# Kernel optimization log

Hardware: AMD Instinct MI355X
Metric: run time of the kernel (lower is better)

The kernel has to match this reference:

```python
import jax, jax.numpy as jnp
import numpy as np
import math

EPS = 1e-6


def setup_inputs() -> dict:
    key = jax.random.key(0)
    ks = jax.random.split(key, 6)
    Bsz, S, d_in, d_out, E, r = 4, 2048, 2048, 2048, 16, 16
    x = jax.random.normal(ks[0], (Bsz, S, d_in), dtype=jnp.float32)
    base_W = jax.random.normal(ks[1], (d_out, d_in), dtype=jnp.float32) * (1.0 / math.sqrt(d_in))
    base_b = jax.random.normal(ks[2], (d_out,), dtype=jnp.float32)
    A = jax.random.normal(ks[3], (E, r, d_in), dtype=jnp.float32) * (1.0 / math.sqrt(d_in))
    B = jax.random.normal(ks[4], (E, d_out, r), dtype=jnp.float32) * (1.0 / math.sqrt(r))
    gate_v = jax.random.normal(ks[5], (E, d_in), dtype=jnp.float32)
    alphas = jnp.full((E,), 32.0, dtype=jnp.float32)
    return {"x": x, "base_W": base_W, "base_b": base_b, "A": A, "B": B,
            "gate_v": gate_v, "alphas": alphas, "top_k": 2}


def reference(x, base_W, base_b, A, B, gate_v, alphas, top_k):
    d = x.shape[-1]
    out_shape = x.shape[:-1] + (base_W.shape[0],)
    base_out = jnp.einsum('bsd,od->bso', x, base_W) + base_b

    x_flat = x.reshape(-1, d)                                  # [T, d]
    T = x_flat.shape[0]
    E = A.shape[0]
    # cosine routing scores
    xn = x_flat / (jnp.linalg.norm(x_flat, axis=-1, keepdims=True) + EPS)
    vn = gate_v / (jnp.linalg.norm(gate_v, axis=-1, keepdims=True) + EPS)
    scores = (xn @ vn.T) / jnp.sqrt(jnp.float32(d))            # [T, E]
    topk_s, topk_i = jax.lax.top_k(scores, top_k)              # [T, k]
    w = jax.nn.softmax(topk_s, axis=-1)                        # [T, k]
    # dense combine weight per (token, expert); non-selected experts get 0
    Wte = jnp.zeros((T, E), dtype=x.dtype).at[jnp.arange(T)[:, None], topk_i].add(w)
    scale = alphas / jnp.float32(A.shape[1])                   # [E]
    # grouped LoRA: mid [T,E,r] is tiny (r=16); contract without [T,E,out]
    mid = jnp.einsum('td,erd->ter', x_flat, A)
    contrib = jnp.einsum('ter,eor,te,e->to', mid, B, Wte, scale)
    return base_out + contrib.reshape(out_shape)
```

## Files before the change

kernel.cpp:

```cpp
#include <hip/hip_runtime.h>
#include <math.h>


typedef unsigned short u16;
typedef __attribute__((ext_vector_type(8))) short short8;
typedef __attribute__((ext_vector_type(4))) float floatx4;

#define DEV __device__ __forceinline__

DEV u16 f2b(float f) { unsigned int u; __builtin_memcpy(&u, &f, 4); u += 0x7fffu + ((u >> 16) & 1u); return (u16)(u >> 16); }
DEV float ldf(const float* __restrict__ p, long long i, long long n) { if (i < 0 || i >= n) i = 0; return p[i]; }

DEV void async_cp16(const void* g, void* l) {
  __builtin_amdgcn_global_load_lds(
      (const __attribute__((address_space(1))) unsigned int*)g,
      (__attribute__((address_space(3))) unsigned int*)l, 16, 0, 0);
}

struct Route { int e0, e1; float c0, c1; };

#define MAX_T 8192
#define MAX_K 2048
#define MAX_DOUT 2048
#define MAX_ER 256

__device__ Route g_route[MAX_T];
__device__ float g_vnorm[16];
__device__ float g_mid[(size_t)MAX_T * MAX_ER];
__device__ __align__(16) u16 g_xb[(size_t)MAX_T * MAX_K];
__device__ __align__(16) u16 g_wb[(size_t)MAX_DOUT * MAX_K];
__device__ __align__(16) u16 g_ab[(size_t)MAX_ER * MAX_K];
__device__ __align__(16) u16 g_mw[(size_t)MAX_T * MAX_ER];
__device__ __align__(16) u16 g_w2[(size_t)MAX_DOUT * MAX_ER];

__global__ __launch_bounds__(256) void prep_all(
    const float* __restrict__ W, long long nW,
    const float* __restrict__ A, long long nA,
    const float* __restrict__ Bw, long long nB,
    const float* __restrict__ gv, long long nG,
    int d, int d_out, int r, int E, int Er,
    int nWblk, int nAblk, int w2blk) {
  int b = blockIdx.x;
  const int tid = threadIdx.x;
  if (b < nWblk) {
    const long long cap = (long long)MAX_DOUT * MAX_K;
    const long long stride = (long long)nWblk * 1024;
    for (long long i4 = ((long long)b * 256 + tid) * 4; i4 < nW; i4 += stride) {
      if (i4 + 4 <= nW && i4 + 4 <= cap) {
        const float4 v = *(const float4*)(W + i4);
        ushort4 o; o.x = f2b(v.x); o.y = f2b(v.y); o.z = f2b(v.z); o.w = f2b(v.w);
        *(ushort4*)&g_wb[i4] = o;
      } else {
        for (long long j = i4; j < nW && j < cap; ++j) g_wb[j] = f2b(W[j]);
      }
    }
    return;
  }
  b -= nWblk;
  if (b < nAblk) {
    const long long cap = (long long)MAX_ER * MAX_K;
    const long long stride = (long long)nAblk * 1024;
    for (long long i4 = ((long long)b * 256 + tid) * 4; i4 < nA; i4 += stride) {
      if (i4 + 4 <= nA && i4 + 4 <= cap) {
        const float4 v = *(const float4*)(A + i4);
        ushort4 o; o.x = f2b(v.x); o.y = f2b(v.y); o.z = f2b(v.z); o.w = f2b(v.w);
        *(ushort4*)&g_ab[i4] = o;
      } else {
        for (long long j = i4; j < nA && j < cap; ++j) g_ab[j] = f2b(A[j]);
      }
    }
    return;
  }
  b -= nAblk;
  if (b < w2blk) {
    const int gid = b * 256 + tid;
    if (gid >= d_out * E) return;
    const int o = gid / E, e = gid % E;
    const long long src = ((long long)e * d_out + o) * r;
    const long long dst = (long long)o * Er + (long long)e * r;
    if (r == 16 && src + 16 <= nB) {
      short8 lo, hi;
#pragma unroll
      for (int j = 0; j < 8; ++j) lo[j] = (short)f2b(Bw[src + j]);
#pragma unroll
      for (int j = 0; j < 8; ++j) hi[j] = (short)f2b(Bw[src + 8 + j]);
      *(short8*)&g_w2[dst] = lo;
      *(short8*)&g_w2[dst + 8] = hi;
    } else {
      for (int j = 0; j < r; ++j) g_w2[dst + j] = f2b(ldf(Bw, src + j, nB));
    }
    return;
  }
  b -= w2blk;
  if (b < E && b < 16 && tid < 64) {
    float vv = 0.f;
    const float* gp = gv + (long long)b * d;
    for (int k = tid * 4; k + 4 <= d; k += 256) {
      const float4 g = *(const float4*)(gp + k);
      vv += g.x * g.x + g.y * g.y + g.z * g.z + g.w * g.w;
    }
#pragma unroll
    for (int m = 1; m < 64; m <<= 1) vv += __shfl_xor(vv, m);
    if (tid == 0) g_vnorm[b] = sqrtf(vv) + 1e-6f;
  }
}

__global__ __launch_bounds__(256) void router_cvtx(
    const float* __restrict__ x, long long nX,
    const float* __restrict__ gate_v, long long nG,
    const float* __restrict__ alphas, long long nAl,
    const int* __restrict__ topk_ptr, int has_topk,
    int T, int d, int r, int E) {
  const int wave = threadIdx.x >> 6, lane = threadIdx.x & 63;
  const int t = blockIdx.x * 4 + wave;
  if (t >= T || t >= MAX_T) return;
  float xx = 0.f, dot[16], vv[16];
#pragma unroll
  for (int e = 0; e < 16; ++e) { dot[e] = 0.f; vv[e] = 0.f; }
  const long long xbase = (long long)t * d;
  const int dvec = ((d & 3) == 0) ? d : 0;
  for (int i = lane * 4; i < dvec; i += 256) {
    const float4 xv = *(const float4*)(x + xbase + i);
    xx += xv.x * xv.x + xv.y * xv.y + xv.z * xv.z + xv.w * xv.w;
    ushort4 ob; ob.x = f2b(xv.x); ob.y = f2b(xv.y); ob.z = f2b(xv.z); ob.w = f2b(xv.w);
    *(ushort4*)&g_xb[xbase + i] = ob;
#pragma unroll
    for (int e = 0; e < 16; ++e) {
      if (e < E) {
        const float4 g = *(const float4*)(gate_v + (long long)e * d + i);
        dot[e] += xv.x * g.x + xv.y * g.y + xv.z * g.z + xv.w * g.w;
        vv[e] += g.x * g.x + g.y * g.y + g.z * g.z + g.w * g.w;
      }
    }
  }
  for (int i = dvec + lane; i < d; i += 64) {
    const float xv = ldf(x, xbase + i, nX);
    g_xb[xbase + i] = f2b(xv);
    xx += xv * xv;
#pragma unroll
    for (int e = 0; e < 16; ++e) {
      if (e < E) {
        const float g = ldf(gate_v, (long long)e * d + i, nG);
        dot[e] += xv * g;
        vv[e] += g * g;
      }
    }
  }
#pragma unroll
  for (int m = 1; m < 64; m <<= 1) {
    xx += __shfl_xor(xx, m);
#pragma unroll
    for (int e = 0; e < 16; ++e) {
      dot[e] += __shfl_xor(dot[e], m);
      vv[e] += __shfl_xor(vv[e], m);
    }
  }
  const float inv_sd = 1.0f / sqrtf((float)d);
  const float xnorm = sqrtf(xx) + 1e-6f;
  float s[16];
#pragma unroll
  for (int e = 0; e < 16; ++e)
    s[e] = (e < E) ? dot[e] / (xnorm * (sqrtf(vv[e]) + 1e-6f)) * inv_sd : -1e30f;
  int e0 = 0; float s0 = s[0];
#pragma unroll
  for (int e = 1; e < 16; ++e) if (s[e] > s0) { s0 = s[e]; e0 = e; }
  int e1 = (e0 == 0) ? 1 : 0; float s1 = s[e1];
#pragma unroll
  for (int e = 0; e < 16; ++e) if (e != e0 && s[e] > s1) { s1 = s[e]; e1 = e; }
  const int k = has_topk ? *topk_ptr : 2;
  float w0 = 1.f, w1 = 0.f;
  if (k >= 2) {
    const float ex = expf(s1 - s0);
    w0 = 1.f / (1.f + ex);
    w1 = ex / (1.f + ex);
  } else {
    e1 = e0;
  }
  if (lane == 0) {
    Route rt;
    rt.e0 = e0; rt.e1 = e1;
    rt.c0 = w0 * ldf(alphas, e0, nAl) / (float)r;
    rt.c1 = w1 * ldf(alphas, e1, nAl) / (float)r;
    g_route[t] = rt;
  }
}

__global__ __launch_bounds__(256) void router_lds(
    const float* __restrict__ x, long long nX,
    const float* __restrict__ gate_v, long long nG,
    const float* __restrict__ alphas, long long nAl,
    const int* __restrict__ topk_ptr, int has_topk,
    int T, int d, int r, int E) {
  __shared__ __align__(16) float gls[4096];
  const int tid = threadIdx.x;
  const int w = tid >> 6, lane = tid & 63;
  const int t = blockIdx.x * 4 + w;
  const bool valid = (t < T && t < MAX_T);
  const long long xbase = (long long)t * d;

  float dot[16], xx = 0.f;
#pragma unroll
  for (int e = 0; e < 16; ++e) dot[e] = 0.f;

  for (int k0 = 0; k0 < d; k0 += 256) {
    __syncthreads();
#pragma unroll
    for (int i = 0; i < 4; ++i) {
      const int f = tid * 4 + i * 1024;
      const int e = f >> 8, kk = f & 255;
      float4 g = (float4){0.f, 0.f, 0.f, 0.f};
      if (e < E) g = *(const float4*)(gate_v + (long long)e * d + k0 + kk);
      *(float4*)&gls[f] = g;
    }
    __syncthreads();
    float4 xv = (float4){0.f, 0.f, 0.f, 0.f};
    if (valid) {
      xv = *(const float4*)(x + xbase + k0 + lane * 4);
      ushort4 ob; ob.x = f2b(xv.x); ob.y = f2b(xv.y); ob.z = f2b(xv.z); ob.w = f2b(xv.w);
      *(ushort4*)&g_xb[xbase + k0 + lane * 4] = ob;
    }
    xx += xv.x * xv.x + xv.y * xv.y + xv.z * xv.z + xv.w * xv.w;
#pragma unroll
    for (int e = 0; e < 16; ++e) {
      if (e < E) {
        const float4 g = *(const float4*)&gls[e * 256 + lane * 4];
        dot[e] += xv.x * g.x + xv.y * g.y + xv.z * g.z + xv.w * g.w;
      }
    }
  }
#pragma unroll
  for (int m = 1; m < 64; m <<= 1) {
    xx += __shfl_xor(xx, m);
#pragma unroll
    for (int e = 0; e < 16; ++e) dot[e] += __shfl_xor(dot[e], m);
  }
  if (valid && lane == 0) {
    const float inv_sd = 1.0f / sqrtf((float)d);
    const float xnorm = sqrtf(xx) + 1e-6f;
    float s[16];
#pragma unroll
    for (int e = 0; e < 16; ++e)
      s[e] = (e < E) ? dot[e] / (xnorm * g_vnorm[e]) * inv_sd : -1e30f;
    int e0 = 0; float s0 = s[0];
#pragma unroll
    for (int e = 1; e < 16; ++e) if (s[e] > s0) { s0 = s[e]; e0 = e; }
    int e1 = (e0 == 0) ? 1 : 0; float s1 = s[e1];
#pragma unroll
    for (int e = 0; e < 16; ++e) if (e != e0 && s[e] > s1) { s1 = s[e]; e1 = e; }
    const int k = has_topk ? *topk_ptr : 2;
    float w0 = 1.f, w1 = 0.f;
    if (k >= 2) {
      const float ex = expf(s1 - s0);
      w0 = 1.f / (1.f + ex);
      w1 = ex / (1.f + ex);
    } else {
      e1 = e0;
    }
    Route rt;
    rt.e0 = e0; rt.e1 = e1;
    rt.c0 = w0 * ldf(alphas, e0, nAl) / (float)r;
    rt.c1 = w1 * ldf(alphas, e1, nAl) / (float)r;
    g_route[t] = rt;
  }
}

#define BM 128
#define BN 128
#define BK 32

__global__ __launch_bounds__(256) void gemm_main(
    const float* __restrict__ bias, long long nBias,
    float* __restrict__ Out, long long nOut,
    int K, int d_out, int Er, int T) {
  __shared__ __align__(16) u16 As[BM * BK];
  __shared__ __align__(16) u16 Bs[BN * BK];
  const int tid = threadIdx.x;
  const int w = tid >> 6, lane = tid & 63;
  const int Mb = blockIdx.y * BM;
  const int Nb = blockIdx.x * BN;
  const int wm = w >> 1, wn = w & 1;
  const int chunk0 = w * 2;
  const int srow = lane >> 2;
  const int kb = (lane & 3) * 8;

  floatx4 acc[4][4];
#pragma unroll
  for (int mt = 0; mt < 4; ++mt)
#pragma unroll
    for (int nt = 0; nt < 4; ++nt) acc[mt][nt] = (floatx4){0.f, 0.f, 0.f, 0.f};

  for (int k0 = 0; k0 < K; k0 += BK) {
#pragma unroll
    for (int c = 0; c < 2; ++c) {
      const int row = (chunk0 + c) * 16 + srow;
      async_cp16(g_xb + (size_t)(Mb + row) * K + (k0 + kb), (char*)As + (chunk0 + c) * 1024);
    }
#pragma unroll
    for (int c = 0; c < 2; ++c) {
      const int row = (chunk0 + c) * 16 + srow;
      const int col = Nb + row;
      const u16* g = (col >= d_out) ? g_ab + (size_t)(col - d_out) * K + (k0 + kb)
                                    : g_wb + (size_t)col * K + (k0 + kb);
      async_cp16(g, (char*)Bs + (chunk0 + c) * 1024);
    }
    __syncthreads();
    short8 a[4], b[4];
#pragma unroll
    for (int mt = 0; mt < 4; ++mt)
      a[mt] = *(const short8*)&As[(wm * 64 + mt * 16 + (lane & 15)) * BK + (lane >> 4) * 8];
#pragma unroll
    for (int nt = 0; nt < 4; ++nt)
      b[nt] = *(const short8*)&Bs[(wn * 64 + nt * 16 + (lane & 15)) * BK + (lane >> 4) * 8];
#pragma unroll
    for (int mt = 0; mt < 4; ++mt)
#pragma unroll
      for (int nt = 0; nt < 4; ++nt)
        acc[mt][nt] = __builtin_amdgcn_mfma_f32_16x16x32_bf16(a[mt], b[nt], acc[mt][nt], 0, 0, 0);
    __syncthreads();
  }

  const int colb = Nb + wn * 64 + (lane & 15);
  const int rowb = Mb + wm * 64 + (lane >> 4) * 4;
#pragma unroll
  for (int nt = 0; nt < 4; ++nt) {
    const int col = colb + nt * 16;
    const bool isOut = (col < d_out);
    const float bv = isOut ? ldf(bias, col, nBias) : 0.f;
#pragma unroll
    for (int mt = 0; mt < 4; ++mt) {
      const int row = rowb + mt * 16;
#pragma unroll
      for (int i = 0; i < 4; ++i) {
        const int rr = row + i;
        if (rr >= T) continue;
        if (isOut) {
          const long long idx = (long long)rr * d_out + col;
          if (idx < nOut) Out[idx] = acc[mt][nt][i] + bv;
        } else {
          const int mc = col - d_out;
          if (mc < Er) g_mid[(long long)rr * Er + mc] = acc[mt][nt][i];
        }
      }
    }
  }
}

__global__ __launch_bounds__(256) void build_mw(int T, int r, int Er, int E) {
  const int t = blockIdx.x;
  if (t >= T) return;
  const Route rt = g_route[t];
  for (int j = threadIdx.x; j < Er; j += 256) {
    const int e = (r == 16) ? (j >> 4) : (j / r);
    float wgt = 0.f;
    if (e == rt.e0) wgt = rt.c0;
    else if (e == rt.e1) wgt = rt.c1;
    g_mw[(long long)t * Er + j] = f2b(wgt * g_mid[(long long)t * Er + j]);
  }
}

__global__ __launch_bounds__(256) void gemm_lora(
    float* __restrict__ Out, long long nOut, int Kc, int d_out, int T) {
  __shared__ __align__(16) u16 As[BM * BK];
  __shared__ __align__(16) u16 Bs[BN * BK];
  const int tid = threadIdx.x;
  const int w = tid >> 6, lane = tid & 63;
  const int Mb = blockIdx.y * BM;
  const int Nb = blockIdx.x * BN;
  const int wm = w >> 1, wn = w & 1;
  const int chunk0 = w * 2;
  const int srow = lane >> 2;
  const int kb = (lane & 3) * 8;

  floatx4 acc[4][4];
#pragma unroll
  for (int mt = 0; mt < 4; ++mt)
#pragma unroll
    for (int nt = 0; nt < 4; ++nt) acc[mt][nt] = (floatx4){0.f, 0.f, 0.f, 0.f};

  for (int k0 = 0; k0 < Kc; k0 += BK) {
#pragma unroll
    for (int c = 0; c < 2; ++c) {
      const int row = (chunk0 + c) * 16 + srow;
      async_cp16(g_mw + (size_t)(Mb + row) * Kc + (k0 + kb), (char*)As + (chunk0 + c) * 1024);
      async_cp16(g_w2 + (size_t)(Nb + row) * Kc + (k0 + kb), (char*)Bs + (chunk0 + c) * 1024);
    }
    __syncthreads();
    short8 a[4], b[4];
#pragma unroll
    for (int mt = 0; mt < 4; ++mt)
      a[mt] = *(const short8*)&As[(wm * 64 + mt * 16 + (lane & 15)) * BK + (lane >> 4) * 8];
#pragma unroll
    for (int nt = 0; nt < 4; ++nt)
      b[nt] = *(const short8*)&Bs[(wn * 64 + nt * 16 + (lane & 15)) * BK + (lane >> 4) * 8];
#pragma unroll
    for (int mt = 0; mt < 4; ++mt)
#pragma unroll
      for (int nt = 0; nt < 4; ++nt)
        acc[mt][nt] = __builtin_amdgcn_mfma_f32_16x16x32_bf16(a[mt], b[nt], acc[mt][nt], 0, 0, 0);
    __syncthreads();
  }

  const int colb = Nb + wn * 64 + (lane & 15);
  const int rowb = Mb + wm * 64 + (lane >> 4) * 4;
#pragma unroll
  for (int nt = 0; nt < 4; ++nt) {
    const int col = colb + nt * 16;
#pragma unroll
    for (int mt = 0; mt < 4; ++mt) {
      const int row = rowb + mt * 16;
#pragma unroll
      for (int i = 0; i < 4; ++i) {
        const int rr = row + i;
        if (rr >= T) continue;
        const long long idx = (long long)rr * d_out + col;
        if (idx < nOut) Out[idx] += acc[mt][nt][i];
      }
    }
  }
}


__global__ __launch_bounds__(256) void gemm_mid64(int K, int Er, int T, int r) {
  __shared__ __align__(16) u16 As[128 * 32];
  __shared__ __align__(16) u16 Bs[64 * 32];
  const int tid = threadIdx.x;
  const int w = tid >> 6, lane = tid & 63;
  int lin = blockIdx.y * gridDim.x + blockIdx.x;
  const int nwg = gridDim.x * gridDim.y;
  if ((nwg & 7) == 0) { const int cpx = nwg >> 3; lin = (lin & 7) * cpx + (lin >> 3); }
  const int Mb = (lin / gridDim.x) * 128;
  const int Nb = (lin % gridDim.x) * 64;
  const int wm = w >> 1, wn = w & 1;
  const int srow = lane >> 2;
  const int kb = (lane & 3) * 8;
  const int lane15 = lane & 15, laneHi = lane >> 4;

  floatx4 acc[4][2];
#pragma unroll
  for (int mt = 0; mt < 4; ++mt)
#pragma unroll
    for (int nt = 0; nt < 2; ++nt) acc[mt][nt] = (floatx4){0.f, 0.f, 0.f, 0.f};

  for (int k0 = 0; k0 < K; k0 += 32) {
#pragma unroll
    for (int c = 0; c < 2; ++c) {
      const int ci = w * 2 + c;
      async_cp16(g_xb + (size_t)(Mb + ci * 16 + srow) * K + (k0 + kb), (char*)As + ci * 1024);
    }
    async_cp16(g_ab + (size_t)(Nb + w * 16 + srow) * K + (k0 + kb), (char*)Bs + w * 1024);
    __syncthreads();
    short8 a[4], b[2];
#pragma unroll
    for (int mt = 0; mt < 4; ++mt)
      a[mt] = *(const short8*)&As[(wm * 64 + mt * 16 + lane15) * 32 + laneHi * 8];
#pragma unroll
    for (int nt = 0; nt < 2; ++nt)
      b[nt] = *(const short8*)&Bs[(wn * 32 + nt * 16 + lane15) * 32 + laneHi * 8];
#pragma unroll
    for (int mt = 0; mt < 4; ++mt)
#pragma unroll
      for (int nt = 0; nt < 2; ++nt)
        acc[mt][nt] = __builtin_amdgcn_mfma_f32_16x16x32_bf16(a[mt], b[nt], acc[mt][nt], 0, 0, 0);
    __syncthreads();
  }

  const int colb = Nb + wn * 32 + lane15;
  const int rowb = Mb + wm * 64 + laneHi * 4;
#pragma unroll
  for (int mt = 0; mt < 4; ++mt) {
#pragma unroll
    for (int i = 0; i < 4; ++i) {
      const int rr = rowb + mt * 16 + i;
      if (rr >= T) continue;
      const Route rt = g_route[rr];
#pragma unroll
      for (int nt = 0; nt < 2; ++nt) {
        const int col = colb + nt * 16;
        if (col >= Er) continue;
        const int e = (r == 16) ? (col >> 4) : (col / r);
        float wgt = 0.f;
        if (e == rt.e0) wgt = rt.c0;
        else if (e == rt.e1) wgt = rt.c1;
        g_mw[(long long)rr * Er + col] = f2b(wgt * acc[mt][nt][i]);
      }
    }
  }
}

DEV void stage_ht(int tsched, int half, int isB, int NT, int Mb, int Nb,
                  int Kxb, int Er, char* smem, int w, int lane) {
  int t = (tsched < NT) ? tsched : (NT - 1);
  const int k0 = t << 6;
  const u16* src; int stride, col0;
  if (k0 < Kxb) { src = isB ? g_wb : g_xb; stride = Kxb; col0 = k0; }
  else          { src = isB ? g_w2 : g_mw; stride = Er;  col0 = k0 - Kxb; }
  const int rbase = (isB ? Nb : Mb) + (half << 7);
  char* dst = smem + (tsched & 1) * 65536 + isB * 32768 + half * 16384 + (w * 2) * 1024;
  const int row = w * 16 + (lane >> 3);
  const int cs = (((lane & 7) ^ (lane >> 3)) << 3);
#pragma unroll
  for (int c = 0; c < 2; ++c) {
    async_cp16(src + (size_t)(rbase + row + c * 8) * stride + col0 + cs, dst + c * 1024);
  }
}

__global__ __launch_bounds__(512, 2) void gemm_main8(
    const float* __restrict__ bias, long long nBias,
    float* __restrict__ Out, long long nOut,
    int Kxb, int d_out, int Er, int T) {
  __shared__ __align__(16) char smem[131072];
  const int tid = threadIdx.x;
  const int w = tid >> 6, lane = tid & 63;
  const int wm = w >> 2, wn = w & 3;
  const int lane15 = lane & 15, laneHi = lane >> 4, lane7 = lane & 7;
  const int NT = (Kxb + Er) >> 6;

  int lin = blockIdx.y * gridDim.x + blockIdx.x;
  const int nwg = gridDim.x * gridDim.y;
  if ((nwg & 7) == 0) { const int cpx = nwg >> 3; lin = (lin & 7) * cpx + (lin >> 3); }
  const int Nb = (lin % gridDim.x) * 256;
  const int Mb = (lin / gridDim.x) * 256;

  floatx4 acc[8][4];
#pragma unroll
  for (int m = 0; m < 8; ++m)
#pragma unroll
    for (int n = 0; n < 4; ++n) acc[m][n] = (floatx4){0.f, 0.f, 0.f, 0.f};

  stage_ht(0, 0, 0, NT, Mb, Nb, Kxb, Er, smem, w, lane);
  stage_ht(0, 1, 0, NT, Mb, Nb, Kxb, Er, smem, w, lane);
  stage_ht(0, 0, 1, NT, Mb, Nb, Kxb, Er, smem, w, lane);
  stage_ht(0, 1, 1, NT, Mb, Nb, Kxb, Er, smem, w, lane);
  stage_ht(1, 0, 1, NT, Mb, Nb, Kxb, Er, smem, w, lane);
  stage_ht(1, 1, 1, NT, Mb, Nb, Kxb, Er, smem, w, lane);
  asm volatile("s_waitcnt vmcnt(4)" ::: "memory");
  __builtin_amdgcn_s_barrier();
  asm volatile("" ::: "memory");

  const int xorw = lane7 << 4;
  short8 a[2][2], b[4][2];

  for (int t = 0; t < NT; ++t) {
    const int sbase = (t & 1) * 65536;
    const char* Ab = smem + sbase;
    const char* Bb = smem + sbase + 32768;
#pragma unroll
    for (int q = 0; q < 4; ++q) {
      if (q == 0) {
#pragma unroll
        for (int n = 0; n < 4; ++n)
#pragma unroll
          for (int kk = 0; kk < 2; ++kk)
            b[n][kk] = *(const short8*)(Bb + (wn * 64 + n * 16 + lane15) * 128 +
                                        ((kk * 64 + laneHi * 16) ^ xorw));
      }
#pragma unroll
      for (int mm = 0; mm < 2; ++mm)
#pragma unroll
        for (int kk = 0; kk < 2; ++kk)
          a[mm][kk] = *(const short8*)(Ab + (wm * 128 + (2 * q + mm) * 16 + lane15) * 128 +
                                       ((kk * 64 + laneHi * 16) ^ xorw));
      if (q < 2) stage_ht(t + 1, q, 0, NT, Mb, Nb, Kxb, Er, smem, w, lane);
      else       stage_ht(t + 2, q - 2, 1, NT, Mb, Nb, Kxb, Er, smem, w, lane);
      if (q == 3) asm volatile("s_waitcnt vmcnt(4)" ::: "memory");
      __builtin_amdgcn_s_barrier();
      asm volatile("" ::: "memory");
      asm volatile("s_waitcnt lgkmcnt(0)" ::: "memory");
      __builtin_amdgcn_s_setprio(1);
#pragma unroll
      for (int kk = 0; kk < 2; ++kk)
#pragma unroll
        for (int mm = 0; mm < 2; ++mm)
#pragma unroll
          for (int n = 0; n < 4; ++n)
            acc[2 * q + mm][n] =
                __builtin_amdgcn_mfma_f32_16x16x32_bf16(a[mm][kk], b[n][kk], acc[2 * q + mm][n], 0, 0, 0);
      __builtin_amdgcn_s_setprio(0);
      __builtin_amdgcn_s_barrier();
      asm volatile("" ::: "memory");
    }
  }
  asm volatile("s_waitcnt vmcnt(0)" ::: "memory");

  const int colb = Nb + wn * 64 + lane15;
  const int rowb = Mb + wm * 128 + laneHi * 4;
#pragma unroll
  for (int n = 0; n < 4; ++n) {
    const int col = colb + n * 16;
    const float bv = ldf(bias, col, nBias);
#pragma unroll
    for (int m = 0; m < 8; ++m) {
#pragma unroll
      for (int i = 0; i < 4; ++i) {
        const int row = rowb + m * 16 + i;
        const long long idx = (long long)row * d_out + col;
        if (row < T && idx < nOut) Out[idx] = acc[m][n][i] + bv;
      }
    }
  }
}

extern "C" void kernel_launch(void* const* d_in, const int* in_sizes, int n_in,
                              void* d_out, int out_size, void* d_ws, size_t ws_size,
                              hipStream_t stream) {
  if (n_in < 7 || !d_out) return;
  const float* x    = (const float*)d_in[0];
  const float* W    = (const float*)d_in[1];
  const float* bias = (const float*)d_in[2];
  const float* A    = (const float*)d_in[3];
  const float* B    = (const float*)d_in[4];
  const float* gv   = (const float*)d_in[5];
  const float* al   = (const float*)d_in[6];
  const int has_topk = (n_in > 7 && in_sizes[7] >= 1) ? 1 : 0;
  const int* topk = has_topk ? (const int*)d_in[7] : nullptr;
  float* out = (float*)d_out;

  const long long nX = in_sizes[0], nW = in_sizes[1], nBias = in_sizes[2];
  const long long nA = in_sizes[3], nB = in_sizes[4], nG = in_sizes[5], nAl = in_sizes[6];
  const long long nOut = (long long)out_size;

  const int E = in_sizes[6] > 0 ? in_sizes[6] : 1;
  int d = (int)(nG / E); if (d < 1) d = 1;
  const int d_out_dim = in_sizes[2] > 0 ? in_sizes[2] : 1;
  int T = (int)(nX / d);
  int r = (int)(nA / ((long long)E * d)); if (r < 1) r = 1;
  const int Er = E * r;
  if (T < 1) return;
  if (T > MAX_T) T = MAX_T;
  if (d > MAX_K || d_out_dim > MAX_DOUT || Er > MAX_ER) return;

  const int nWblk = 2048, nAblk = 256;
  const int w2blk = (d_out_dim * E + 255) / 256;
  prep_all<<<nWblk + nAblk + w2blk + E, 256, 0, stream>>>(
      W, nW, A, nA, B, nB, gv, nG, d, d_out_dim, r, E, Er, nWblk, nAblk, w2blk);

  const bool fastr = (d % 256 == 0) && (E <= 16);
  if (fastr)
    router_lds<<<(T + 3) / 4, 256, 0, stream>>>(x, nX, gv, nG, al, nAl, topk, has_topk, T, d, r, E);
  else
    router_cvtx<<<(T + 3) / 4, 256, 0, stream>>>(x, nX, gv, nG, al, nAl, topk, has_topk, T, d, r, E);

  const bool fast = (T % 256 == 0) && (d_out_dim % 256 == 0) && (d % 64 == 0) &&
                    (Er % 64 == 0) && (((d + Er) >> 6) >= 2) && (Er >= 64);
  if (fast) {
    dim3 gmid(Er / 64, T / 128);
    gemm_mid64<<<gmid, 256, 0, stream>>>(d, Er, T, r);
    dim3 gmain(d_out_dim / 256, T / 256);
    gemm_main8<<<gmain, 512, 0, stream>>>(bias, nBias, out, nOut, d, d_out_dim, Er, T);
  } else {
    dim3 grid1((d_out_dim + Er + BN - 1) / BN, (T + BM - 1) / BM);
    gemm_main<<<grid1, 256, 0, stream>>>(bias, nBias, out, nOut, d, d_out_dim, Er, T);
    build_mw<<<T, 256, 0, stream>>>(T, r, Er, E);
    dim3 grid2((d_out_dim + BN - 1) / BN, (T + BM - 1) / BM);
    gemm_lora<<<grid2, 256, 0, stream>>>(out, nOut, Er, d_out_dim, T);
  }
}
```

Before: 300.3 us.

## Fuse router into weight-prep kernel with double-buffered gate tiles and inline vnorm

Merges the LDS router kernel into the weight conversion kernel as extra blocks in one launch, so routing runs alongside the bf16 conversion of W, A and B. The router now computes the gate-vector norms itself instead of reading g_vnorm, which removes the dependency on a separate norm pass. It also double-buffers the gate_v tiles in LDS, cutting the synchronisation per chunk from two barriers to one. The aim is to save a launch and overlap two memory-bound phases. The cost is doubled LDS use per block, which may lower occupancy for the conversion blocks that share the kernel, plus redundant norm work in every router block.

```diff
diff --git a/kernel.cpp b/kernel.cpp
--- a/kernel.cpp
+++ b/kernel.cpp
@@ -25,7 +25,6 @@
 #define MAX_ER 256
 
 __device__ Route g_route[MAX_T];
-__device__ float g_vnorm[16];
 __device__ float g_mid[(size_t)MAX_T * MAX_ER];
 __device__ __align__(16) u16 g_xb[(size_t)MAX_T * MAX_K];
 __device__ __align__(16) u16 g_wb[(size_t)MAX_DOUT * MAX_K];
@@ -33,15 +32,122 @@
 __device__ __align__(16) u16 g_mw[(size_t)MAX_T * MAX_ER];
 __device__ __align__(16) u16 g_w2[(size_t)MAX_DOUT * MAX_ER];
 
-__global__ __launch_bounds__(256) void prep_all(
+__global__ __launch_bounds__(256) void router_prep(
+    const float* __restrict__ x, long long nX,
+    const float* __restrict__ gate_v, long long nG,
+    const float* __restrict__ alphas, long long nAl,
+    const int* __restrict__ topk_ptr, int has_topk,
     const float* __restrict__ W, long long nW,
     const float* __restrict__ A, long long nA,
     const float* __restrict__ Bw, long long nB,
-    const float* __restrict__ gv, long long nG,
-    int d, int d_out, int r, int E, int Er,
-    int nWblk, int nAblk, int w2blk) {
+    int T, int d, int d_out, int r, int E, int Er,
+    int Rblk, int nWblk, int nAblk, int w2blk) {
+  __shared__ __align__(16) float gls[2][4096];
+  __shared__ float vns[16];
   int b = blockIdx.x;
   const int tid = threadIdx.x;
+
+  if (b < Rblk) {
+    const int w = tid >> 6, lane = tid & 63;
+    const int t = b * 4 + w;
+    const bool valid = (t < T && t < MAX_T);
+    const long long xbase = (long long)t * d;
+    const int nch = d >> 8;
+
+    float dot[16], xx = 0.f, vvp[4] = {0.f, 0.f, 0.f, 0.f};
+#pragma unroll
+    for (int e = 0; e < 16; ++e) dot[e] = 0.f;
+
+#pragma unroll
+    for (int i = 0; i < 4; ++i) {
+      const int f = tid * 4 + i * 1024;
+      const int e = f >> 8, kk = f & 255;
+      float4 g = (float4){0.f, 0.f, 0.f, 0.f};
+      if (e < E) g = *(const float4*)(gate_v + (long long)e * d + kk);
+      vvp[i] += g.x * g.x + g.y * g.y + g.z * g.z + g.w * g.w;
+      *(float4*)&gls[0][f] = g;
+    }
+    __syncthreads();
+
+    for (int j = 0; j < nch; ++j) {
+      if (j + 1 < nch) {
+        const int k1 = (j + 1) << 8;
+#pragma unroll
+        for (int i = 0; i < 4; ++i) {
+          const int f = tid * 4 + i * 1024;
+          const int e = f >> 8, kk = f & 255;
+          float4 g = (float4){0.f, 0.f, 0.f, 0.f};
+          if (e < E) g = *(const float4*)(gate_v + (long long)e * d + k1 + kk);
+          vvp[i] += g.x * g.x + g.y * g.y + g.z * g.z + g.w * g.w;
+          *(float4*)&gls[(j + 1) & 1][f] = g;
+        }
+      }
+      const int k0 = j << 8;
+      float4 xv = (float4){0.f, 0.f, 0.f, 0.f};
+      if (valid) {
+        xv = *(const float4*)(x + xbase + k0 + lane * 4);
+        ushort4 ob; ob.x = f2b(xv.x); ob.y = f2b(xv.y); ob.z = f2b(xv.z); ob.w = f2b(xv.w);
+        *(ushort4*)&g_xb[xbase + k0 + lane * 4] = ob;
+      }
+      xx += xv.x * xv.x + xv.y * xv.y + xv.z * xv.z + xv.w * xv.w;
+      const float* gb = gls[j & 1];
+#pragma unroll
+      for (int e = 0; e < 16; ++e) {
+        if (e < E) {
+          const float4 g = *(const float4*)&gb[e * 256 + lane * 4];
+          dot[e] += xv.x * g.x + xv.y * g.y + xv.z * g.z + xv.w * g.w;
+        }
+      }
+      __syncthreads();
+    }
+
+#pragma unroll
+    for (int m = 1; m < 64; m <<= 1)
+#pragma unroll
+      for (int i = 0; i < 4; ++i) vvp[i] += __shfl_xor(vvp[i], m);
+    if (lane == 0) {
+#pragma unroll
+      for (int i = 0; i < 4; ++i) vns[w + 4 * i] = sqrtf(vvp[i]) + 1e-6f;
+    }
+#pragma unroll
+    for (int m = 1; m < 64; m <<= 1) {
+      xx += __shfl_xor(xx, m);
+#pragma unroll
+      for (int e = 0; e < 16; ++e) dot[e] += __shfl_xor(dot[e], m);
+    }
+    __syncthreads();
+    if (valid && lane == 0) {
+      const float inv_sd = 1.0f / sqrtf((float)d);
+      const float xnorm = sqrtf(xx) + 1e-6f;
+      float s[16];
+#pragma unroll
+      for (int e = 0; e < 16; ++e)
+        s[e] = (e < E) ? dot[e] / (xnorm * vns[e]) * inv_sd : -1e30f;
+      int e0 = 0; float s0 = s[0];
+#pragma unroll
+      for (int e = 1; e < 16; ++e) if (s[e] > s0) { s0 = s[e]; e0 = e; }
+      int e1 = (e0 == 0) ? 1 : 0; float s1 = s[e1];
+#pragma unroll
+      for (int e = 0; e < 16; ++e) if (e != e0 && s[e] > s1) { s1 = s[e]; e1 = e; }
+      const int k = has_topk ? *topk_ptr : 2;
+      float w0 = 1.f, w1 = 0.f;
+      if (k >= 2) {
+        const float ex = expf(s1 - s0);
+        w0 = 1.f / (1.f + ex);
+        w1 = ex / (1.f + ex);
+      } else {
+        e1 = e0;
+      }
+      Route rt;
+      rt.e0 = e0; rt.e1 = e1;
+      rt.c0 = w0 * ldf(alphas, e0, nAl) / (float)r;
+      rt.c1 = w1 * ldf(alphas, e1, nAl) / (float)r;
+      g_route[t] = rt;
+    }
+    return;
+  }
+  b -= Rblk;
+
   if (b < nWblk) {
     const long long cap = (long long)MAX_DOUT * MAX_K;
     const long long stride = (long long)nWblk * 1024;
@@ -89,19 +195,6 @@
     } else {
       for (int j = 0; j < r; ++j) g_w2[dst + j] = f2b(ldf(Bw, src + j, nB));
     }
-    return;
-  }
-  b -= w2blk;
-  if (b < E && b < 16 && tid < 64) {
-    float vv = 0.f;
-    const float* gp = gv + (long long)b * d;
-    for (int k = tid * 4; k + 4 <= d; k += 256) {
-      const float4 g = *(const float4*)(gp + k);
-      vv += g.x * g.x + g.y * g.y + g.z * g.z + g.w * g.w;
-    }
-#pragma unroll
-    for (int m = 1; m < 64; m <<= 1) vv += __shfl_xor(vv, m);
-    if (tid == 0) g_vnorm[b] = sqrtf(vv) + 1e-6f;
   }
 }
 
@@ -177,85 +270,6 @@
     e1 = e0;
   }
   if (lane == 0) {
-    Route rt;
-    rt.e0 = e0; rt.e1 = e1;
-    rt.c0 = w0 * ldf(alphas, e0, nAl) / (float)r;
-    rt.c1 = w1 * ldf(alphas, e1, nAl) / (float)r;
-    g_route[t] = rt;
-  }
-}
-
-__global__ __launch_bounds__(256) void router_lds(
-    const float* __restrict__ x, long long nX,
-    const float* __restrict__ gate_v, long long nG,
-    const float* __restrict__ alphas, long long nAl,
-    const int* __restrict__ topk_ptr, int has_topk,
-    int T, int d, int r, int E) {
-  __shared__ __align__(16) float gls[4096];
-  const int tid = threadIdx.x;
-  const int w = tid >> 6, lane = tid & 63;
-  const int t = blockIdx.x * 4 + w;
-  const bool valid = (t < T && t < MAX_T);
-  const long long xbase = (long long)t * d;
-
-  float dot[16], xx = 0.f;
-#pragma unroll
-  for (int e = 0; e < 16; ++e) dot[e] = 0.f;
-
-  for (int k0 = 0; k0 < d; k0 += 256) {
-    __syncthreads();
-#pragma unroll
-    for (int i = 0; i < 4; ++i) {
-      const int f = tid * 4 + i * 1024;
-      const int e = f >> 8, kk = f & 255;
-      float4 g = (float4){0.f, 0.f, 0.f, 0.f};
-      if (e < E) g = *(const float4*)(gate_v + (long long)e * d + k0 + kk);
-      *(float4*)&gls[f] = g;
-    }
-    __syncthreads();
-    float4 xv = (float4){0.f, 0.f, 0.f, 0.f};
-    if (valid) {
-      xv = *(const float4*)(x + xbase + k0 + lane * 4);
-      ushort4 ob; ob.x = f2b(xv.x); ob.y = f2b(xv.y); ob.z = f2b(xv.z); ob.w = f2b(xv.w);
-      *(ushort4*)&g_xb[xbase + k0 + lane * 4] = ob;
-    }
-    xx += xv.x * xv.x + xv.y * xv.y + xv.z * xv.z + xv.w * xv.w;
-#pragma unroll
-    for (int e = 0; e < 16; ++e) {
-      if (e < E) {
-        const float4 g = *(const float4*)&gls[e * 256 + lane * 4];
-        dot[e] += xv.x * g.x + xv.y * g.y + xv.z * g.z + xv.w * g.w;
-      }
-    }
-  }
-#pragma unroll
-  for (int m = 1; m < 64; m <<= 1) {
-    xx += __shfl_xor(xx, m);
-#pragma unroll
-    for (int e = 0; e < 16; ++e) dot[e] += __shfl_xor(dot[e], m);
-  }
-  if (valid && lane == 0) {
-    const float inv_sd = 1.0f / sqrtf((float)d);
-    const float xnorm = sqrtf(xx) + 1e-6f;
-    float s[16];
-#pragma unroll
-    for (int e = 0; e < 16; ++e)
-      s[e] = (e < E) ? dot[e] / (xnorm * g_vnorm[e]) * inv_sd : -1e30f;
-    int e0 = 0; float s0 = s[0];
-#pragma unroll
-    for (int e = 1; e < 16; ++e) if (s[e] > s0) { s0 = s[e]; e0 = e; }
-    int e1 = (e0 == 0) ? 1 : 0; float s1 = s[e1];
-#pragma unroll
-    for (int e = 0; e < 16; ++e) if (e != e0 && s[e] > s1) { s1 = s[e]; e1 = e; }
-    const int k = has_topk ? *topk_ptr : 2;
-    float w0 = 1.f, w1 = 0.f;
-    if (k >= 2) {
-      const float ex = expf(s1 - s0);
-      w0 = 1.f / (1.f + ex);
-      w1 = ex / (1.f + ex);
-    } else {
-      e1 = e0;
-    }
     Route rt;
     rt.e0 = e0; rt.e1 = e1;
     rt.c0 = w0 * ldf(alphas, e0, nAl) / (float)r;
@@ -629,15 +643,16 @@
   if (T > MAX_T) T = MAX_T;
   if (d > MAX_K || d_out_dim > MAX_DOUT || Er > MAX_ER) return;
 
+  const bool fastr = (d % 256 == 0) && (E <= 16);
+  const int Rblk = fastr ? (T + 3) / 4 : 0;
   const int nWblk = 2048, nAblk = 256;
   const int w2blk = (d_out_dim * E + 255) / 256;
-  prep_all<<<nWblk + nAblk + w2blk + E, 256, 0, stream>>>(
-      W, nW, A, nA, B, nB, gv, nG, d, d_out_dim, r, E, Er, nWblk, nAblk, w2blk);
-
-  const bool fastr = (d % 256 == 0) && (E <= 16);
-  if (fastr)
-    router_lds<<<(T + 3) / 4, 256, 0, stream>>>(x, nX, gv, nG, al, nAl, topk, has_topk, T, d, r, E);
-  else
+
+  router_prep<<<Rblk + nWblk + nAblk + w2blk, 256, 0, stream>>>(
+      x, nX, gv, nG, al, nAl, topk, has_topk,
+      W, nW, A, nA, B, nB,
+      T, d, d_out_dim, r, E, Er, Rblk, nWblk, nAblk, w2blk);
+  if (!fastr)
     router_cvtx<<<(T + 3) / 4, 256, 0, stream>>>(x, nX, gv, nG, al, nAl, topk, has_topk, T, d, r, E);
 
   const bool fast = (T % 256 == 0) && (d_out_dim % 256 == 0) && (d % 64 == 0) &&
```

Result: no change. 306.2 us (+2.0%).
